# Kernel tuning notes

Hardware: AMD Instinct MI355X
Metric: run time of the kernel (lower is better)

The kernel has to match this reference:

```python
import jax, jax.numpy as jnp
import numpy as np
import math

N_EMB = 256
N_HEAD = 8
B_SEGS = 128
T_SEG = 256  # equal-length segments; N = B_SEGS * T_SEG


def setup_inputs() -> dict:
    key = jax.random.key(0)
    ks = jax.random.split(key, 10)
    N = B_SEGS * T_SEG
    x = jax.random.normal(ks[0], (N, N_EMB), dtype=jnp.float32)
    batch = jnp.repeat(jnp.arange(B_SEGS, dtype=jnp.int64), T_SEG)
    s = 1.0 / math.sqrt(N_EMB)
    def lin(k):
        kw, kb = jax.random.split(k)
        W = jax.random.uniform(kw, (N_EMB, N_EMB), jnp.float32, -s, s)
        b = jax.random.uniform(kb, (N_EMB,), jnp.float32, -s, s)
        return W, b
    Wq, bq = lin(ks[1])
    Wk, bk = lin(ks[2])
    Wv, bv = lin(ks[3])
    Wp, bp = lin(ks[4])
    return {"x": x, "batch": batch, "Wq": Wq, "bq": bq, "Wk": Wk, "bk": bk,
            "Wv": Wv, "bv": bv, "Wp": Wp, "bp": bp}


def reference(x, batch, Wq, bq, Wk, bk, Wv, bv, Wp, bp):
    # Dropout layers are identity in eval / p=0.
    N, C = x.shape
    H = N_HEAD
    hd = C // H
    B = int(batch[-1]) + 1        # equal-length segments
    T = N // B
    xr = x.reshape(B, T, C)
    # per-segment QKV projections: [B,H,T,hd]
    def heads(W, b):
        return (xr @ W.T + b).reshape(B, T, H, hd).transpose(0, 2, 1, 3)
    q = heads(Wq, bq)
    k = heads(Wk, bk)
    v = heads(Wv, bv)
    scores = jnp.einsum('bhtd,bhsd->bhts', q, k) * (1.0 / math.sqrt(hd))
    attn = jax.nn.softmax(scores, axis=-1)          # [B,H,T,T]
    y = jnp.einsum('bhts,bhsd->bhtd', attn, v)      # [B,H,T,hd]
    y = y.transpose(0, 2, 1, 3).reshape(B, T, C)
    y = y @ Wp.T + bp
    attn_mean = attn.mean(axis=1)                   # head-mean per segment [B,T,T]
    return y.reshape(N, C), attn_mean
```

## Files before the change

### kernel.cpp

```cpp
#include <hip/hip_runtime.h>
#include <hip/hip_bf16.h>
#include <stdint.h>

typedef unsigned short u16;
typedef __bf16 bf16_t;
typedef bf16_t bf16x8 __attribute__((ext_vector_type(8)));
typedef float f32x4 __attribute__((ext_vector_type(4)));

#define NTOK 32768
#define CEMB 256
#define NHEAD 8
#define HD 32
#define BSEG 128
#define TSEG 256

#define SCQ (0.17677669529663687f * 1.4426950408889634f)

static __device__ __forceinline__ bf16x8 ld16(const u16* p) {
  uint4 v = *reinterpret_cast<const uint4*>(p);
  return __builtin_bit_cast(bf16x8, v);
}
static __device__ __forceinline__ u16 f2b(float f) {
  return __builtin_bit_cast(u16, (bf16_t)f);
}

typedef __attribute__((address_space(1))) const void GASV;
typedef __attribute__((address_space(3))) void LASV;
static __device__ __forceinline__ void stage16(const u16* g, u16* l) {
  __builtin_amdgcn_global_load_lds((GASV*)g, (LASV*)l, 16, 0, 0);
}

__global__ void k_convert(const float* __restrict__ x,
                          const float* __restrict__ wq, const float* __restrict__ wk,
                          const float* __restrict__ wv, const float* __restrict__ wp,
                          u16* __restrict__ xb, u16* __restrict__ wb) {
  const int XSLOTS = (NTOK * CEMB) / 8;
  const int WSLOTS = (4 * CEMB * CEMB) / 8;
  int slot = blockIdx.x * blockDim.x + threadIdx.x;
  if (slot >= XSLOTS + WSLOTS) return;
  const float* src;
  u16* dst;
  if (slot < XSLOTS) {
    src = x + slot * 8;
    dst = xb + slot * 8;
  } else {
    int e = (slot - XSLOTS) * 8;
    int wsel = e >> 16, off = e & 65535;
    const float* s0 = (wsel == 0) ? wq : ((wsel == 1) ? wk : ((wsel == 2) ? wv : wp));
    src = s0 + off;
    dst = wb + e;
  }
  float4 a = reinterpret_cast<const float4*>(src)[0];
  float4 b = reinterpret_cast<const float4*>(src)[1];
  u16 o[8] = {f2b(a.x), f2b(a.y), f2b(a.z), f2b(a.w),
              f2b(b.x), f2b(b.y), f2b(b.z), f2b(b.w)};
  *reinterpret_cast<uint4*>(dst) = *reinterpret_cast<const uint4*>(o);
}

#define GEMM_MAIN_LOOP(Asrc, Bsrc)                                              \
  f32x4 acc[4][4];                                                              \
  _Pragma("unroll") for (int mf = 0; mf < 4; ++mf)                              \
      _Pragma("unroll") for (int nf = 0; nf < 4; ++nf) {                        \
    f32x4 z = {0.f, 0.f, 0.f, 0.f};                                             \
    acc[mf][nf] = z;                                                            \
  }                                                                             \
  u16* As = lds;                                                                \
  u16* Bs = lds + 16384;                                                        \
  auto STAGE = [&](int buf, int kt) {                                           \
    _Pragma("unroll") for (int i = 0; i < 4; ++i) {                             \
      int cidx = i * 256 + tid;                                                 \
      int row = cidx >> 3;                                                      \
      int scb = ((cidx & 7) << 4) ^ ((row & 7) << 4);        \
      u16* dst_lds = As + buf * 8192 + (i * 256 + w * 64) * 8;                  \
      stage16(Asrc + (size_t)(m0 + row) * CEMB + kt * 64 + (scb >> 1), dst_lds);\
      u16* dst_ldsb = Bs + buf * 8192 + (i * 256 + w * 64) * 8;                 \
      stage16(Bsrc + (size_t)(n0 + row) * CEMB + kt * 64 + (scb >> 1), dst_ldsb);\
    }                                                                           \
  };                                                                            \
  STAGE(0, 0);                                                                  \
  __syncthreads();                                                              \
  for (int kt = 0; kt < 4; ++kt) {                                              \
    int buf = kt & 1;                                                           \
    if (kt < 3) STAGE(buf ^ 1, kt + 1);                                         \
    bf16x8 av[4][2], bw[4][2];                                                  \
    _Pragma("unroll") for (int mf = 0; mf < 4; ++mf)                            \
        _Pragma("unroll") for (int kk = 0; kk < 2; ++kk) {                      \
      int row = wr * 64 + mf * 16 + lr;                                         \
      int byte = row * 128 + ((kk * 64 + lg * 16) ^ ((row & 7) << 4));          \
      av[mf][kk] = *reinterpret_cast<const bf16x8*>(                            \
          (const char*)(As + buf * 8192) + byte);                               \
    }                                                                           \
    _Pragma("unroll") for (int nf = 0; nf < 4; ++nf)                            \
        _Pragma("unroll") for (int kk = 0; kk < 2; ++kk) {                      \
      int row = wc * 64 + nf * 16 + lr;                                         \
      int byte = row * 128 + ((kk * 64 + lg * 16) ^ ((row & 7) << 4));          \
      bw[nf][kk] = *reinterpret_cast<const bf16x8*>(                            \
          (const char*)(Bs + buf * 8192) + byte);                               \
    }                                                                           \
    _Pragma("unroll") for (int kk = 0; kk < 2; ++kk)                            \
        _Pragma("unroll") for (int nf = 0; nf < 4; ++nf)                        \
            _Pragma("unroll") for (int mf = 0; mf < 4; ++mf)                    \
      acc[mf][nf] = __builtin_amdgcn_mfma_f32_16x16x32_bf16(                    \
          av[mf][kk], bw[nf][kk], acc[mf][nf], 0, 0, 0);                        \
    __syncthreads();                                                            \
  }

__global__ __launch_bounds__(256, 2)
void k_qkv(const u16* __restrict__ xb, const u16* __restrict__ wb,
           const float* __restrict__ bq, const float* __restrict__ bk,
           const float* __restrict__ bv,
           u16* __restrict__ q_ws, u16* __restrict__ k_ws, u16* __restrict__ v_ws) {
  const int d = blockIdx.x;
  const int xcd = d & 7, i = d >> 3;
  const int m_idx = xcd * 32 + i / 6;
  const int rr = i % 6;
  const int mode = rr >> 1;
  const int n0 = (rr & 1) * 128;
  const int m0 = m_idx * 128;
  const int tid = threadIdx.x;
  const int w = tid >> 6, l = tid & 63;
  const int lr = l & 15, lg = l >> 4;
  const int wr = w >> 1, wc = w & 1;

  __shared__ u16 lds[32768];

  const u16* W = wb + mode * (CEMB * CEMB);
  const float* bias = (mode == 0) ? bq : ((mode == 1) ? bk : bv);

  GEMM_MAIN_LOOP(xb, W)

  float bb[4];
#pragma unroll
  for (int nf = 0; nf < 4; ++nf) bb[nf] = bias[n0 + wc * 64 + nf * 16 + lr];

  const float osc = (mode == 0) ? SCQ : 1.0f;

  if (mode < 2) {
    u16* Et = lds;
#pragma unroll
    for (int mf = 0; mf < 4; ++mf)
#pragma unroll
      for (int nf = 0; nf < 4; ++nf)
#pragma unroll
        for (int r = 0; r < 4; ++r) {
          int row = wr * 64 + mf * 16 + lg * 4 + r;
          int col = wc * 64 + nf * 16 + lr;
          int byte = (row * 256 + col * 2) ^ ((row & 7) << 4);
          *(u16*)((char*)Et + byte) = f2b((acc[mf][nf][r] + bb[nf]) * osc);
        }
    __syncthreads();
    u16* out = (mode == 0) ? q_ws : k_ws;
    int row_l = tid >> 1, half = tid & 1;
    u16* dstp = out + (size_t)(m0 + row_l) * CEMB + n0 + half * 64;
#pragma unroll
    for (int j = 0; j < 8; ++j) {
      int byte = row_l * 256 + (((half * 64 + j * 8) * 2) ^ ((row_l & 7) << 4));
      *reinterpret_cast<uint4*>(dstp + j * 8) =
          *reinterpret_cast<const uint4*>((const char*)Et + byte);
    }
  } else {
    u16* Vt = lds;
#pragma unroll
    for (int mf = 0; mf < 4; ++mf)
#pragma unroll
      for (int nf = 0; nf < 4; ++nf)
#pragma unroll
        for (int r = 0; r < 4; ++r) {
          int row = wr * 64 + mf * 16 + lg * 4 + r;
          int col = wc * 64 + nf * 16 + lr;
          int byte = (col * 256 + row * 2) ^ ((col & 7) << 4);
          *(u16*)((char*)Vt + byte) = f2b(acc[mf][nf][r] + bb[nf]);
        }
    __syncthreads();
    int col_l = tid >> 1, half = tid & 1;
    int c = n0 + col_l, hh = c >> 5, dd = c & 31;
    int bs = m0 >> 8, t0 = m0 & 255;
    u16* dst = v_ws + ((size_t)(bs * NHEAD + hh) * HD + dd) * TSEG + t0 + half * 64;
#pragma unroll
    for (int j = 0; j < 8; ++j) {
      int byte = col_l * 256 + ((half * 128 + j * 16) ^ ((col_l & 7) << 4));
      *reinterpret_cast<uint4*>(dst + j * 8) =
          *reinterpret_cast<const uint4*>((const char*)Vt + byte);
    }
  }
}

__global__ __launch_bounds__(1024, 4)
void k_attn(const u16* __restrict__ q_ws, const u16* __restrict__ k_ws,
            const u16* __restrict__ v_ws, const u16* __restrict__ wb,
            const float* __restrict__ bp,
            float* __restrict__ out, float* __restrict__ mean_out) {
  const int dblk = blockIdx.x;
  const int xcd = dblk & 7, ii = dblk >> 3;
  const int b = xcd * 16 + (ii >> 1);
  const int th = ii & 1;
  const int tid = threadIdx.x;
  const int w = tid >> 6, l = tid & 63;
  const int lr = l & 15, lg = l >> 4;
  const int wt = w & 7, sh = w >> 3;
  const int tbase = th * 128 + wt * 16;

  extern __shared__ u16 ldsKV[];
  float* smb = reinterpret_cast<float*>(ldsKV + 32768);
  float* ylds = reinterpret_cast<float*>(ldsKV + 33280);
  char* yTile = reinterpret_cast<char*>(ldsKV) + 83968;

  float macc[8][4];
#pragma unroll
  for (int st = 0; st < 8; ++st)
#pragma unroll
    for (int r = 0; r < 4; ++r) macc[st][r] = 0.f;

  const u16* qseg = q_ws + (size_t)b * TSEG * CEMB;
  const u16* kseg = k_ws + (size_t)b * TSEG * CEMB;
  const u16* vseg = v_ws + (size_t)(b * NHEAD) * HD * TSEG;

  auto STAGE_KV = [&](int hn, int bn) {
    int idx = tid;
    int c = idx >> 6, l2 = idx & 63;
    int lr2 = l2 & 15, lg2 = l2 >> 4;
    int srow = 32 * (c >> 1) + 4 * (c & 1) + 8 * (lr2 >> 2) + (lr2 & 3);
    stage16(kseg + srow * CEMB + hn * HD + lg2 * 8, ldsKV + (bn * 1024 + idx) * 8);
    int vrow = (c >> 3) * 16 + lr2;
    int vcol = (c & 7) * 32 + lg2 * 8;
    stage16(vseg + (size_t)(hn * HD + vrow) * TSEG + vcol,
            ldsKV + 16384 + (bn * 1024 + idx) * 8);
  };

  STAGE_KV(0, 0);
  bf16x8 qf = ld16(qseg + (tbase + lr) * CEMB + lg * 8);

  const int own_slot = wt * 2 + sh;
  const int par_slot = wt * 2 + (1 - sh);

  for (int h = 0; h < NHEAD; ++h) {
    const int bn = h & 1;
    __syncthreads();
    if (h < 7) STAGE_KV(h + 1, bn ^ 1);
    const u16* Kb = ldsKV + bn * 8192;
    const u16* Vb = ldsKV + 16384 + bn * 8192;

    float s[8][4];
#pragma unroll
    for (int st = 0; st < 8; ++st) {
      bf16x8 kf = *reinterpret_cast<const bf16x8*>(Kb + ((sh * 8 + st) * 64 + l) * 8);
      f32x4 z = {0.f, 0.f, 0.f, 0.f};
      f32x4 dd = __builtin_amdgcn_mfma_f32_16x16x32_bf16(kf, qf, z, 0, 0, 0);
#pragma unroll
      for (int r = 0; r < 4; ++r) s[st][r] = dd[r];
    }

    qf = ld16(qseg + (tbase + lr) * CEMB + ((h + 1) & 7) * HD + lg * 8);

    float s0 = 0.f, s1 = 0.f, s2 = 0.f, s3 = 0.f;
#pragma unroll
    for (int st = 0; st < 8; ++st) {
      float p0 = exp2f(s[st][0]);
      float p1 = exp2f(s[st][1]);
      float p2 = exp2f(s[st][2]);
      float p3 = exp2f(s[st][3]);
      s[st][0] = p0; s[st][1] = p1; s[st][2] = p2; s[st][3] = p3;
      s0 += p0; s1 += p1; s2 += p2; s3 += p3;
    }
    float sm = (s0 + s1) + (s2 + s3);
    sm += __shfl_xor(sm, 16, 64);
    sm += __shfl_xor(sm, 32, 64);

    bf16x8 pb[4];
#pragma unroll
    for (int kk = 0; kk < 4; ++kk)
#pragma unroll
      for (int e = 0; e < 4; ++e) {
        pb[kk][e] = (bf16_t)s[2 * kk][e];
        pb[kk][4 + e] = (bf16_t)s[2 * kk + 1][e];
      }

    f32x4 y0 = {0.f, 0.f, 0.f, 0.f}, y1 = {0.f, 0.f, 0.f, 0.f};
#pragma unroll
    for (int kk = 0; kk < 4; ++kk) {
      bf16x8 vf0 = *reinterpret_cast<const bf16x8*>(Vb + ((0 * 8 + sh * 4 + kk) * 64 + l) * 8);
      bf16x8 vf1 = *reinterpret_cast<const bf16x8*>(Vb + ((1 * 8 + sh * 4 + kk) * 64 + l) * 8);
      y0 = __builtin_amdgcn_mfma_f32_16x16x32_bf16(vf0, pb[kk], y0, 0, 0, 0);
      y1 = __builtin_amdgcn_mfma_f32_16x16x32_bf16(vf1, pb[kk], y1, 0, 0, 0);
    }

    if (l < 16) smb[own_slot * 16 + l] = sm;
    {
      f32x4 ywr = (sh == 0) ? y1 : y0;
      *reinterpret_cast<f32x4*>(ylds + own_slot * 272 + lg * 68 + lr * 4) = ywr;
    }

    __builtin_amdgcn_sched_barrier(0);
    asm volatile("s_waitcnt lgkmcnt(0)" ::: "memory");
    __builtin_amdgcn_s_barrier();
    __builtin_amdgcn_sched_barrier(0);

    float smT = sm + smb[par_slot * 16 + lr];
    float inv = __builtin_amdgcn_rcpf(smT);

#pragma unroll
    for (int st = 0; st < 8; ++st)
#pragma unroll
      for (int r = 0; r < 4; ++r)
        macc[st][r] = fmaf(s[st][r], inv, macc[st][r]);

    {
      f32x4 ymine = (sh == 0) ? y0 : y1;
      f32x4 ypar = *reinterpret_cast<const f32x4*>(ylds + par_slot * 272 + lg * 68 + lr * 4);
      u16 o[4];
#pragma unroll
      for (int r = 0; r < 4; ++r) o[r] = f2b((ymine[r] + ypar[r]) * inv);
      int row = wt * 16 + lr;
      int colb = h * 64 + sh * 32 + lg * 8;
      *reinterpret_cast<uint2*>(yTile + row * 512 + (colb ^ ((row & 7) << 4))) =
          *reinterpret_cast<const uint2*>(o);
    }
  }

  __syncthreads();

  {
    float* smem = reinterpret_cast<float*>(ldsKV);
    float* smw = smem + w * (16 * 65) + lr * 65;
    const int trow = l >> 2;
    const int cql = (l & 3) * 4;
    const float* srcp = smem + w * (16 * 65) + trow * 65 + cql;
    float* gdst = mean_out + (size_t)(b * TSEG + tbase + trow) * TSEG + sh * 128 + cql;
    for (int c = 0; c < 2; ++c) {
#pragma unroll
      for (int j = 0; j < 4; ++j) {
        int st = 4 * c + j;
        int sl = 32 * ((st >> 1) & 1) + 4 * (st & 1) + 8 * lg;
#pragma unroll
        for (int r = 0; r < 4; ++r) smw[sl + r] = macc[st][r] * 0.125f;
      }
#pragma unroll
      for (int j = 0; j < 4; ++j)
        *reinterpret_cast<f32x4*>(gdst + c * 64 + j * 16) =
            *reinterpret_cast<const f32x4*>(srcp + j * 16);
    }
  }
  __syncthreads();

  {
    const u16* wbP = wb + 3 * (CEMB * CEMB);
    const int wrP = w >> 2, wcP = w & 3;

    auto STAGE_W = [&](int kt, int bn) {
      u16* Wb = ldsKV + bn * 16384;
#pragma unroll
      for (int r = 0; r < 2; ++r) {
        int cidx = (r * 16 + w) * 64 + l;
        int row = cidx >> 3;
        int scb = ((cidx & 7) << 4) ^ ((row & 7) << 4);
        stage16(wbP + (size_t)row * CEMB + kt * 64 + (scb >> 1),
                Wb + (r * 16 + w) * 512);
      }
    };

    f32x4 acc[2][4];
#pragma unroll
    for (int mf = 0; mf < 2; ++mf)
#pragma unroll
      for (int nf = 0; nf < 4; ++nf) {
        f32x4 z = {0.f, 0.f, 0.f, 0.f};
        acc[mf][nf] = z;
      }

    STAGE_W(0, 0);
    __syncthreads();
    for (int kt = 0; kt < 4; ++kt) {
      int buf = kt & 1;
      if (kt < 3) STAGE_W(kt + 1, buf ^ 1);
      const char* Wb = (const char*)(ldsKV + buf * 16384);
      bf16x8 av[2][2], bw[4][2];
#pragma unroll
      for (int mf = 0; mf < 2; ++mf)
#pragma unroll
        for (int kk = 0; kk < 2; ++kk) {
          int row = wrP * 32 + mf * 16 + lr;
          int byte = row * 512 + ((kt * 128 + kk * 64 + lg * 16) ^ ((row & 7) << 4));
          av[mf][kk] = *reinterpret_cast<const bf16x8*>(yTile + byte);
        }
#pragma unroll
      for (int nf = 0; nf < 4; ++nf)
#pragma unroll
        for (int kk = 0; kk < 2; ++kk) {
          int row = wcP * 64 + nf * 16 + lr;
          int byte = row * 128 + ((kk * 64 + lg * 16) ^ ((row & 7) << 4));
          bw[nf][kk] = *reinterpret_cast<const bf16x8*>(Wb + byte);
        }
#pragma unroll
      for (int kk = 0; kk < 2; ++kk)
#pragma unroll
        for (int nf = 0; nf < 4; ++nf)
#pragma unroll
          for (int mf = 0; mf < 2; ++mf)
            acc[mf][nf] = __builtin_amdgcn_mfma_f32_16x16x32_bf16(
                av[mf][kk], bw[nf][kk], acc[mf][nf], 0, 0, 0);
      __syncthreads();
    }

    float bb[4];
#pragma unroll
    for (int nf = 0; nf < 4; ++nf) bb[nf] = bp[wcP * 64 + nf * 16 + lr];
#pragma unroll
    for (int mf = 0; mf < 2; ++mf)
#pragma unroll
      for (int nf = 0; nf < 4; ++nf)
#pragma unroll
        for (int r = 0; r < 4; ++r) {
          int m = b * TSEG + th * 128 + wrP * 32 + mf * 16 + lg * 4 + r;
          int c = wcP * 64 + nf * 16 + lr;
          out[(size_t)m * CEMB + c] = acc[mf][nf][r] + bb[nf];
        }
  }
}

extern "C" void kernel_launch(void* const* d_in, const int* in_sizes, int n_in,
                              void* d_out, int out_size, void* d_ws, size_t ws_size,
                              hipStream_t stream) {
  (void)in_sizes; (void)n_in; (void)out_size; (void)ws_size;
  const float* x  = (const float*)d_in[0];
  const float* Wq = (const float*)d_in[2];
  const float* bq = (const float*)d_in[3];
  const float* Wk = (const float*)d_in[4];
  const float* bk = (const float*)d_in[5];
  const float* Wv = (const float*)d_in[6];
  const float* bv = (const float*)d_in[7];
  const float* Wp = (const float*)d_in[8];
  const float* bp = (const float*)d_in[9];
  float* out = (float*)d_out;

  char* ws = (char*)d_ws;
  u16* xb   = (u16*)(ws);
  u16* wb   = (u16*)(ws + 16777216);
  u16* q_ws = (u16*)(ws + 17301504);
  u16* k_ws = (u16*)(ws + 34078720);
  u16* v_ws = (u16*)(ws + 50855936);
  float* mean_out = out + (size_t)NTOK * CEMB;

  k_convert<<<4224, 256, 0, stream>>>(x, Wq, Wk, Wv, Wp, xb, wb);
  k_qkv<<<1536, 256, 0, stream>>>(xb, wb, bq, bk, bv, q_ws, k_ws, v_ws);
  k_attn<<<256, 1024, 149504, stream>>>(q_ws, k_ws, v_ws, wb, bp, out, mean_out);
}
```

Measured before the change: 84.60 us.

## Fuse fp32-to-bf16 conversion into QKV and projection GEMMs, drop convert kernel

Removes the separate conversion kernel. The QKV kernel now loads fp32 x and weights directly, converts them to bf16 in registers and writes them to LDS. It is restructured so one 1024-thread block holds a full 128-row x tile and computes Q, K and V in sequence, with weight tiles double-buffered through registers. The attention kernel likewise converts Wp from fp32 on the fly, which saves the extra launch and the xb round trip through memory. In exchange, each block re-reads and re-converts the fp32 weights, the launch has fewer blocks, and the kernel uses more LDS and more synchronisation.

```diff
diff --git a/kernel.cpp b/kernel.cpp
--- a/kernel.cpp
+++ b/kernel.cpp
@@ -23,6 +23,11 @@
 static __device__ __forceinline__ u16 f2b(float f) {
   return __builtin_bit_cast(u16, (bf16_t)f);
 }
+static __device__ __forceinline__ uint4 cvt8(float4 a, float4 b) {
+  u16 o[8] = {f2b(a.x), f2b(a.y), f2b(a.z), f2b(a.w),
+              f2b(b.x), f2b(b.y), f2b(b.z), f2b(b.w)};
+  return *reinterpret_cast<const uint4*>(o);
+}
 
 typedef __attribute__((address_space(1))) const void GASV;
 typedef __attribute__((address_space(3))) void LASV;
@@ -30,164 +35,178 @@
   __builtin_amdgcn_global_load_lds((GASV*)g, (LASV*)l, 16, 0, 0);
 }
 
-__global__ void k_convert(const float* __restrict__ x,
-                          const float* __restrict__ wq, const float* __restrict__ wk,
-                          const float* __restrict__ wv, const float* __restrict__ wp,
-                          u16* __restrict__ xb, u16* __restrict__ wb) {
-  const int XSLOTS = (NTOK * CEMB) / 8;
-  const int WSLOTS = (4 * CEMB * CEMB) / 8;
-  int slot = blockIdx.x * blockDim.x + threadIdx.x;
-  if (slot >= XSLOTS + WSLOTS) return;
-  const float* src;
-  u16* dst;
-  if (slot < XSLOTS) {
-    src = x + slot * 8;
-    dst = xb + slot * 8;
-  } else {
-    int e = (slot - XSLOTS) * 8;
-    int wsel = e >> 16, off = e & 65535;
-    const float* s0 = (wsel == 0) ? wq : ((wsel == 1) ? wk : ((wsel == 2) ? wv : wp));
-    src = s0 + off;
-    dst = wb + e;
-  }
-  float4 a = reinterpret_cast<const float4*>(src)[0];
-  float4 b = reinterpret_cast<const float4*>(src)[1];
-  u16 o[8] = {f2b(a.x), f2b(a.y), f2b(a.z), f2b(a.w),
-              f2b(b.x), f2b(b.y), f2b(b.z), f2b(b.w)};
-  *reinterpret_cast<uint4*>(dst) = *reinterpret_cast<const uint4*>(o);
-}
-
-#define GEMM_MAIN_LOOP(Asrc, Bsrc)                                              \
-  f32x4 acc[4][4];                                                              \
-  _Pragma("unroll") for (int mf = 0; mf < 4; ++mf)                              \
-      _Pragma("unroll") for (int nf = 0; nf < 4; ++nf) {                        \
-    f32x4 z = {0.f, 0.f, 0.f, 0.f};                                             \
-    acc[mf][nf] = z;                                                            \
-  }                                                                             \
-  u16* As = lds;                                                                \
-  u16* Bs = lds + 16384;                                                        \
-  auto STAGE = [&](int buf, int kt) {                                           \
-    _Pragma("unroll") for (int i = 0; i < 4; ++i) {                             \
-      int cidx = i * 256 + tid;                                                 \
-      int row = cidx >> 3;                                                      \
-      int scb = ((cidx & 7) << 4) ^ ((row & 7) << 4);        \
-      u16* dst_lds = As + buf * 8192 + (i * 256 + w * 64) * 8;                  \
-      stage16(Asrc + (size_t)(m0 + row) * CEMB + kt * 64 + (scb >> 1), dst_lds);\
-      u16* dst_ldsb = Bs + buf * 8192 + (i * 256 + w * 64) * 8;                 \
-      stage16(Bsrc + (size_t)(n0 + row) * CEMB + kt * 64 + (scb >> 1), dst_ldsb);\
-    }                                                                           \
-  };                                                                            \
-  STAGE(0, 0);                                                                  \
-  __syncthreads();                                                              \
-  for (int kt = 0; kt < 4; ++kt) {                                              \
-    int buf = kt & 1;                                                           \
-    if (kt < 3) STAGE(buf ^ 1, kt + 1);                                         \
-    bf16x8 av[4][2], bw[4][2];                                                  \
-    _Pragma("unroll") for (int mf = 0; mf < 4; ++mf)                            \
-        _Pragma("unroll") for (int kk = 0; kk < 2; ++kk) {                      \
-      int row = wr * 64 + mf * 16 + lr;                                         \
-      int byte = row * 128 + ((kk * 64 + lg * 16) ^ ((row & 7) << 4));          \
-      av[mf][kk] = *reinterpret_cast<const bf16x8*>(                            \
-          (const char*)(As + buf * 8192) + byte);                               \
-    }                                                                           \
-    _Pragma("unroll") for (int nf = 0; nf < 4; ++nf)                            \
-        _Pragma("unroll") for (int kk = 0; kk < 2; ++kk) {                      \
-      int row = wc * 64 + nf * 16 + lr;                                         \
-      int byte = row * 128 + ((kk * 64 + lg * 16) ^ ((row & 7) << 4));          \
-      bw[nf][kk] = *reinterpret_cast<const bf16x8*>(                            \
-          (const char*)(Bs + buf * 8192) + byte);                               \
-    }                                                                           \
-    _Pragma("unroll") for (int kk = 0; kk < 2; ++kk)                            \
-        _Pragma("unroll") for (int nf = 0; nf < 4; ++nf)                        \
-            _Pragma("unroll") for (int mf = 0; mf < 4; ++mf)                    \
-      acc[mf][nf] = __builtin_amdgcn_mfma_f32_16x16x32_bf16(                    \
-          av[mf][kk], bw[nf][kk], acc[mf][nf], 0, 0, 0);                        \
-    __syncthreads();                                                            \
-  }
-
-__global__ __launch_bounds__(256, 2)
-void k_qkv(const u16* __restrict__ xb, const u16* __restrict__ wb,
+__global__ __launch_bounds__(1024, 4)
+void k_qkv(const float* __restrict__ x,
+           const float* __restrict__ Wq, const float* __restrict__ Wk,
+           const float* __restrict__ Wv,
            const float* __restrict__ bq, const float* __restrict__ bk,
            const float* __restrict__ bv,
            u16* __restrict__ q_ws, u16* __restrict__ k_ws, u16* __restrict__ v_ws) {
   const int d = blockIdx.x;
-  const int xcd = d & 7, i = d >> 3;
-  const int m_idx = xcd * 32 + i / 6;
-  const int rr = i % 6;
-  const int mode = rr >> 1;
-  const int n0 = (rr & 1) * 128;
+  const int m_idx = (d & 7) * 32 + (d >> 3);
   const int m0 = m_idx * 128;
   const int tid = threadIdx.x;
   const int w = tid >> 6, l = tid & 63;
   const int lr = l & 15, lg = l >> 4;
-  const int wr = w >> 1, wc = w & 1;
-
-  __shared__ u16 lds[32768];
-
-  const u16* W = wb + mode * (CEMB * CEMB);
-  const float* bias = (mode == 0) ? bq : ((mode == 1) ? bk : bv);
-
-  GEMM_MAIN_LOOP(xb, W)
-
-  float bb[4];
-#pragma unroll
-  for (int nf = 0; nf < 4; ++nf) bb[nf] = bias[n0 + wc * 64 + nf * 16 + lr];
-
-  const float osc = (mode == 0) ? SCQ : 1.0f;
-
-  if (mode < 2) {
-    u16* Et = lds;
-#pragma unroll
-    for (int mf = 0; mf < 4; ++mf)
+  const int wrP = w >> 2, wcP = w & 3;
+
+  extern __shared__ char lds[];
+  char* Bs = lds + 65536;
+  char* bounce = lds + 98304;
+
+  const int brow = tid >> 2;
+  const int bcb = (tid & 3) * 2;
+  float4 breg[2][4];
+  auto BLOAD = [&](int bi, float4* r4) {
+    const float* Wsel = (bi >> 2) == 0 ? Wq : ((bi >> 2) == 1 ? Wk : Wv);
+    const float* s = Wsel + (size_t)brow * CEMB + (bi & 3) * 64 + bcb * 8;
+    r4[0] = reinterpret_cast<const float4*>(s)[0];
+    r4[1] = reinterpret_cast<const float4*>(s)[1];
+    r4[2] = reinterpret_cast<const float4*>(s)[2];
+    r4[3] = reinterpret_cast<const float4*>(s)[3];
+  };
+  auto BWRITE = [&](const float4* r4) {
+#pragma unroll
+    for (int jj = 0; jj < 2; ++jj) {
+      int byte = brow * 128 + (((bcb + jj) * 16) ^ ((brow & 7) << 4));
+      *reinterpret_cast<uint4*>(Bs + byte) = cvt8(r4[jj * 2], r4[jj * 2 + 1]);
+    }
+  };
+
+  BLOAD(0, breg[0]);
+  {
+    int row = tid >> 3, seg = tid & 7;
+    const float* src = x + (size_t)(m0 + row) * CEMB + seg * 32;
+#pragma unroll
+    for (int j = 0; j < 4; ++j) {
+      float4 a = reinterpret_cast<const float4*>(src)[2 * j];
+      float4 b = reinterpret_cast<const float4*>(src)[2 * j + 1];
+      int byte = row * 512 + ((seg * 64 + j * 16) ^ ((row & 7) << 4));
+      *reinterpret_cast<uint4*>(lds + byte) = cvt8(a, b);
+    }
+  }
+  BWRITE(breg[0]);
+  BLOAD(1, breg[1]);
+  __syncthreads();
+
+#pragma unroll
+  for (int mode = 0; mode < 3; ++mode) {
+    f32x4 acc[2][4];
+#pragma unroll
+    for (int mf = 0; mf < 2; ++mf)
+#pragma unroll
+      for (int nf = 0; nf < 4; ++nf) {
+        f32x4 z = {0.f, 0.f, 0.f, 0.f};
+        acc[mf][nf] = z;
+      }
+
+#pragma unroll
+    for (int kt = 0; kt < 4; ++kt) {
+      const int bi = mode * 4 + kt;
+      bf16x8 av[2][2], bw[4][2];
+#pragma unroll
+      for (int mf = 0; mf < 2; ++mf)
+#pragma unroll
+        for (int kk = 0; kk < 2; ++kk) {
+          int row = wrP * 32 + mf * 16 + lr;
+          int byte = row * 512 + ((kt * 128 + kk * 64 + lg * 16) ^ ((row & 7) << 4));
+          av[mf][kk] = *reinterpret_cast<const bf16x8*>(lds + byte);
+        }
 #pragma unroll
       for (int nf = 0; nf < 4; ++nf)
 #pragma unroll
-        for (int r = 0; r < 4; ++r) {
-          int row = wr * 64 + mf * 16 + lg * 4 + r;
-          int col = wc * 64 + nf * 16 + lr;
-          int byte = (row * 256 + col * 2) ^ ((row & 7) << 4);
-          *(u16*)((char*)Et + byte) = f2b((acc[mf][nf][r] + bb[nf]) * osc);
-        }
-    __syncthreads();
-    u16* out = (mode == 0) ? q_ws : k_ws;
-    int row_l = tid >> 1, half = tid & 1;
-    u16* dstp = out + (size_t)(m0 + row_l) * CEMB + n0 + half * 64;
-#pragma unroll
-    for (int j = 0; j < 8; ++j) {
-      int byte = row_l * 256 + (((half * 64 + j * 8) * 2) ^ ((row_l & 7) << 4));
-      *reinterpret_cast<uint4*>(dstp + j * 8) =
-          *reinterpret_cast<const uint4*>((const char*)Et + byte);
-    }
-  } else {
-    u16* Vt = lds;
-#pragma unroll
-    for (int mf = 0; mf < 4; ++mf)
-#pragma unroll
-      for (int nf = 0; nf < 4; ++nf)
-#pragma unroll
-        for (int r = 0; r < 4; ++r) {
-          int row = wr * 64 + mf * 16 + lg * 4 + r;
-          int col = wc * 64 + nf * 16 + lr;
-          int byte = (col * 256 + row * 2) ^ ((col & 7) << 4);
-          *(u16*)((char*)Vt + byte) = f2b(acc[mf][nf][r] + bb[nf]);
-        }
-    __syncthreads();
-    int col_l = tid >> 1, half = tid & 1;
-    int c = n0 + col_l, hh = c >> 5, dd = c & 31;
-    int bs = m0 >> 8, t0 = m0 & 255;
-    u16* dst = v_ws + ((size_t)(bs * NHEAD + hh) * HD + dd) * TSEG + t0 + half * 64;
-#pragma unroll
-    for (int j = 0; j < 8; ++j) {
-      int byte = col_l * 256 + ((half * 128 + j * 16) ^ ((col_l & 7) << 4));
-      *reinterpret_cast<uint4*>(dst + j * 8) =
-          *reinterpret_cast<const uint4*>((const char*)Vt + byte);
+        for (int kk = 0; kk < 2; ++kk) {
+          int row = wcP * 64 + nf * 16 + lr;
+          int byte = row * 128 + ((kk * 64 + lg * 16) ^ ((row & 7) << 4));
+          bw[nf][kk] = *reinterpret_cast<const bf16x8*>(Bs + byte);
+        }
+#pragma unroll
+      for (int kk = 0; kk < 2; ++kk)
+#pragma unroll
+        for (int nf = 0; nf < 4; ++nf)
+#pragma unroll
+          for (int mf = 0; mf < 2; ++mf)
+            acc[mf][nf] = __builtin_amdgcn_mfma_f32_16x16x32_bf16(
+                av[mf][kk], bw[nf][kk], acc[mf][nf], 0, 0, 0);
+      __syncthreads();
+      if (bi < 11) {
+        BWRITE(breg[(bi + 1) & 1]);
+        if (bi < 10) BLOAD(bi + 2, breg[bi & 1]);
+        __syncthreads();
+      }
+    }
+
+    const float* bias = (mode == 0) ? bq : ((mode == 1) ? bk : bv);
+    float bb[4];
+#pragma unroll
+    for (int nf = 0; nf < 4; ++nf) bb[nf] = bias[wcP * 64 + nf * 16 + lr];
+
+    if (mode < 2) {
+      const float osc = (mode == 0) ? SCQ : 1.0f;
+      u16* outp = (mode == 0) ? q_ws : k_ws;
+#pragma unroll
+      for (int g = 0; g < 2; ++g) {
+        if ((wrP >> 1) == g) {
+#pragma unroll
+          for (int mf = 0; mf < 2; ++mf)
+#pragma unroll
+            for (int nf = 0; nf < 4; ++nf)
+#pragma unroll
+              for (int r = 0; r < 4; ++r) {
+                int lrow = (wrP & 1) * 32 + mf * 16 + lg * 4 + r;
+                int col = wcP * 64 + nf * 16 + lr;
+                int byte = lrow * 512 + ((col * 2) ^ ((lrow & 7) << 4));
+                *(u16*)(bounce + byte) = f2b((acc[mf][nf][r] + bb[nf]) * osc);
+              }
+        }
+        __syncthreads();
+#pragma unroll
+        for (int jj = 0; jj < 2; ++jj) {
+          int ch = tid * 2 + jj;
+          int crow = ch >> 5, cc = ch & 31;
+          int byte = crow * 512 + ((cc * 16) ^ ((crow & 7) << 4));
+          *reinterpret_cast<uint4*>(outp + (size_t)(m0 + g * 64 + crow) * CEMB + cc * 8) =
+              *reinterpret_cast<const uint4*>(bounce + byte);
+        }
+        __syncthreads();
+      }
+    } else {
+      const int bs = m0 >> 8, t0 = m0 & 255;
+#pragma unroll
+      for (int g = 0; g < 2; ++g) {
+        if ((wcP >> 1) == g) {
+#pragma unroll
+          for (int mf = 0; mf < 2; ++mf)
+#pragma unroll
+            for (int nf = 0; nf < 4; ++nf)
+#pragma unroll
+              for (int r = 0; r < 4; ++r) {
+                int row = wrP * 32 + mf * 16 + lg * 4 + r;
+                int ccol = (wcP & 1) * 64 + nf * 16 + lr;
+                int byte = ccol * 256 + ((row * 2) ^ ((ccol & 7) << 4));
+                *(u16*)(bounce + byte) = f2b(acc[mf][nf][r] + bb[nf]);
+              }
+        }
+        __syncthreads();
+#pragma unroll
+        for (int jj = 0; jj < 2; ++jj) {
+          int ch = tid * 2 + jj;
+          int ccl = ch >> 4, cc = ch & 15;
+          int byte = ccl * 256 + ((cc * 16) ^ ((ccl & 7) << 4));
+          int c = g * 128 + ccl, hh = c >> 5, dd = c & 31;
+          *reinterpret_cast<uint4*>(
+              v_ws + ((size_t)(bs * NHEAD + hh) * HD + dd) * TSEG + t0 + cc * 8) =
+              *reinterpret_cast<const uint4*>(bounce + byte);
+        }
+        __syncthreads();
+      }
     }
   }
 }
 
 __global__ __launch_bounds__(1024, 4)
 void k_attn(const u16* __restrict__ q_ws, const u16* __restrict__ k_ws,
-            const u16* __restrict__ v_ws, const u16* __restrict__ wb,
+            const u16* __restrict__ v_ws, const float* __restrict__ Wp,
             const float* __restrict__ bp,
             float* __restrict__ out, float* __restrict__ mean_out) {
   const int dblk = blockIdx.x;
@@ -319,6 +338,27 @@
 
   __syncthreads();
 
+  const int wrow = tid >> 2;
+  const int wcb = (tid & 3) * 2;
+  float4 wreg[2][4];
+  auto WLOAD = [&](int kt, float4* r4) {
+    const float* s = Wp + (size_t)wrow * CEMB + kt * 64 + wcb * 8;
+    r4[0] = reinterpret_cast<const float4*>(s)[0];
+    r4[1] = reinterpret_cast<const float4*>(s)[1];
+    r4[2] = reinterpret_cast<const float4*>(s)[2];
+    r4[3] = reinterpret_cast<const float4*>(s)[3];
+  };
+  auto WWRITE = [&](const float4* r4, int bn) {
+#pragma unroll
+    for (int jj = 0; jj < 2; ++jj) {
+      int byte = bn * 32768 + wrow * 128 + (((wcb + jj) * 16) ^ ((wrow & 7) << 4));
+      *reinterpret_cast<uint4*>(reinterpret_cast<char*>(ldsKV) + byte) =
+          cvt8(r4[jj * 2], r4[jj * 2 + 1]);
+    }
+  };
+
+  WLOAD(0, wreg[0]);
+
   {
     float* smem = reinterpret_cast<float*>(ldsKV);
     float* smw = smem + w * (16 * 65) + lr * 65;
@@ -343,20 +383,11 @@
   __syncthreads();
 
   {
-    const u16* wbP = wb + 3 * (CEMB * CEMB);
     const int wrP = w >> 2, wcP = w & 3;
 
-    auto STAGE_W = [&](int kt, int bn) {
-      u16* Wb = ldsKV + bn * 16384;
-#pragma unroll
-      for (int r = 0; r < 2; ++r) {
-        int cidx = (r * 16 + w) * 64 + l;
-        int row = cidx >> 3;
-        int scb = ((cidx & 7) << 4) ^ ((row & 7) << 4);
-        stage16(wbP + (size_t)row * CEMB + kt * 64 + (scb >> 1),
-                Wb + (r * 16 + w) * 512);
-      }
-    };
+    WWRITE(wreg[0], 0);
+    WLOAD(1, wreg[1]);
+    __syncthreads();
 
     f32x4 acc[2][4];
 #pragma unroll
@@ -367,12 +398,12 @@
         acc[mf][nf] = z;
       }
 
-    STAGE_W(0, 0);
-    __syncthreads();
+#pragma unroll
     for (int kt = 0; kt < 4; ++kt) {
       int buf = kt & 1;
-      if (kt < 3) STAGE_W(kt + 1, buf ^ 1);
-      const char* Wb = (const char*)(ldsKV + buf * 16384);
+      if (kt < 3) WWRITE(wreg[(kt + 1) & 1], buf ^ 1);
+      if (kt < 2) WLOAD(kt + 2, wreg[kt & 1]);
+      const char* Wb = reinterpret_cast<const char*>(ldsKV) + buf * 32768;
       bf16x8 av[2][2], bw[4][2];
 #pragma unroll
       for (int mf = 0; mf < 2; ++mf)
@@ -433,14 +464,11 @@
   float* out = (float*)d_out;
 
   char* ws = (char*)d_ws;
-  u16* xb   = (u16*)(ws);
-  u16* wb   = (u16*)(ws + 16777216);
-  u16* q_ws = (u16*)(ws + 17301504);
-  u16* k_ws = (u16*)(ws + 34078720);
-  u16* v_ws = (u16*)(ws + 50855936);
+  u16* q_ws = (u16*)(ws);
+  u16* k_ws = (u16*)(ws + 16777216);
+  u16* v_ws = (u16*)(ws + 33554432);
   float* mean_out = out + (size_t)NTOK * CEMB;
 
-  k_convert<<<4224, 256, 0, stream>>>(x, Wq, Wk, Wv, Wp, xb, wb);
-  k_qkv<<<1536, 256, 0, stream>>>(xb, wb, bq, bk, bv, q_ws, k_ws, v_ws);
-  k_attn<<<256, 1024, 149504, stream>>>(q_ws, k_ws, v_ws, wb, bp, out, mean_out);
-}
+  k_qkv<<<256, 1024, 131072, stream>>>(x, Wq, Wk, Wv, bq, bk, bv, q_ws, k_ws, v_ws);
+  k_attn<<<256, 1024, 149504, stream>>>(q_ws, k_ws, v_ws, Wp, bp, out, mean_out);
+}
```

Result: no change. 83.48 us (-1.3%).
